# Performance work log

Hardware: AMD Instinct MI355X
Metric: run time of the kernel (lower is better)

The kernel has to match this reference:

```python
import jax, jax.numpy as jnp
import numpy as np

KEEP_PROB = 0.3
KH, KW = 3, 3
STRIDE = (1, 1)
PADDING = ((1, 1), (1, 1))
DILATION = (1, 1)


def setup_inputs() -> dict:
    key = jax.random.key(0)
    k_x, k_w, k_m, k_b = jax.random.split(key, 4)
    B, C_in, H, W = 16, 64, 112, 112
    C_out = 128
    K = C_in * KH * KW  # 576
    x = jax.random.normal(k_x, (B, C_in, H, W), dtype=jnp.float32)
    weight = jax.random.normal(k_w, (C_out, K), dtype=jnp.float32)
    # binary sparsity pattern of the COO tensor, as a float mask
    mask = (jax.random.uniform(k_m, (C_out, K)) < KEEP_PROB).astype(jnp.float32)
    bias = jax.random.normal(k_b, (C_out,), dtype=jnp.float32)
    return {"x": x, "weight": weight, "mask": mask, "bias": bias}


def reference(x, weight, mask, bias):
    # Effective sparse weight matrix [C_out, C_in*kH*kW]
    spW = weight * mask
    # im2col (F.unfold): patches -> [B, C_in*kH*kW, H_out, W_out]
    # ordering of the K axis is (c, i, j) channel-major, matching torch unfold
    patches = jax.lax.conv_general_dilated_patches(
        x,
        filter_shape=(KH, KW),
        window_strides=STRIDE,
        padding=PADDING,
        rhs_dilation=DILATION,
    )  # [B, K, H_out, W_out]
    # sparse.mm(spW, X) + fold(1x1)  ==  GEMM over the K axis
    out = jnp.einsum('ok,bkhw->bohw', spW, patches)
    out = out + bias[None, :, None, None]
    return out
```

## Files before the change

### kernel.cpp

```cpp
#include <hip/hip_runtime.h>
#include <hip/hip_bf16.h>

#define C_IN    64
#define C_OUT   128
#define HH      112
#define WW      112
#define NB      16
#define KTOT    576
#define NSTEPS  36
#define NPIX    (HH*WW)
#define PH      114
#define PPIX    (PH*PH)
#define XT_OFF  147456
#define XT_BYTES ((size_t)NB * PPIX * C_IN * 2)
#define TILE_H  16
#define TILE_W  16
#define HB_X    18
#define HB_P    324
#define A_BYTES 73728
#define B_BYTES 49152
#define TY      8
#define TX      16
#define HALO_X  18
#define HALO_P  180
#define TILES_X 7
#define NTILES  98

typedef __bf16 bf16x8 __attribute__((ext_vector_type(8)));
typedef float  f32x16 __attribute__((ext_vector_type(16)));

static __device__ __forceinline__ unsigned short f2bf(float v) {
    unsigned int u = __builtin_bit_cast(unsigned int, v);
    u = u + 0x7fffu + ((u >> 16) & 1u);
    return (unsigned short)(u >> 16);
}

__global__ __launch_bounds__(256) void pack_w_kernel(
        const float* __restrict__ weight, const float* __restrict__ mask,
        unsigned short* __restrict__ pw) {
    int t  = blockIdx.x;
    int mt = threadIdx.x >> 6;
    int l  = threadIdx.x & 63;
    int g  = l >> 5;
    int m  = mt * 32 + (l & 31);
    unsigned int words[4];
    #pragma unroll
    for (int ew = 0; ew < 4; ++ew) {
        unsigned int w2[2];
        #pragma unroll
        for (int h = 0; h < 2; ++h) {
            int e    = ew * 2 + h;
            int klog = t * 16 + g * 8 + e;
            int ij   = klog >> 6;
            int c    = klog & 63;
            int ko   = c * 9 + ij;
            w2[h] = f2bf(weight[m * KTOT + ko] * mask[m * KTOT + ko]);
        }
        words[ew] = w2[0] | (w2[1] << 16);
    }
    uint4 o4; o4.x = words[0]; o4.y = words[1]; o4.z = words[2]; o4.w = words[3];
    ((uint4*)pw)[(t * 4 + mt) * 64 + l] = o4;
}

__global__ __launch_bounds__(256) void transpose_x_kernel(
        const float* __restrict__ x, unsigned short* __restrict__ xT) {
    const int b  = blockIdx.y;
    const int pp = blockIdx.x * 256 + threadIdx.x;
    if (pp >= PPIX) return;
    const int hp = pp / PH, wp = pp - hp * PH;
    const int gh = hp - 1, gw = wp - 1;
    const bool valid = (unsigned)gh < (unsigned)HH && (unsigned)gw < (unsigned)WW;
    const float* src = x + (size_t)b * C_IN * (HH * WW) + (gh * WW + gw);
    uint4* dst = (uint4*)(xT + ((size_t)b * PPIX + pp) * C_IN);
    #pragma unroll
    for (int cb = 0; cb < 8; ++cb) {
        unsigned int w4[4];
        #pragma unroll
        for (int h = 0; h < 4; ++h) {
            float v0 = valid ? src[(size_t)(cb * 8 + h * 2    ) * (HH * WW)] : 0.0f;
            float v1 = valid ? src[(size_t)(cb * 8 + h * 2 + 1) * (HH * WW)] : 0.0f;
            w4[h] = (unsigned)f2bf(v0) | ((unsigned)f2bf(v1) << 16);
        }
        uint4 o; o.x = w4[0]; o.y = w4[1]; o.z = w4[2]; o.w = w4[3];
        dst[cb] = o;
    }
}

__global__ __launch_bounds__(512, 2) void sparse_conv_mega_kernel(
        const unsigned short* __restrict__ xT, const unsigned short* __restrict__ pw,
        const float* __restrict__ bias, float* __restrict__ out) {
    __shared__ __align__(16) unsigned char smem[A_BYTES + B_BYTES];
    unsigned char* As = smem;
    unsigned char* Bs = smem + A_BYTES;

    const int bid = (blockIdx.x & 7) * 28 + (blockIdx.x >> 3);
    const int b   = bid / 14;
    const int rem = bid % 14;
    const int mh  = rem & 1;
    const int wx  = rem >> 1;
    const int w0  = wx * TILE_W;
    const int tid = threadIdx.x;
    const int wave = tid >> 6, l = tid & 63;
    const int g = l >> 5, ln = l & 31;

    const char* xTb = (const char*)xT + (size_t)b * PPIX * (C_IN * 2);

    {
        const char* pwb = (const char*)pw;
        #pragma unroll
        for (int r = 0; r < 9; ++r) {
            int c  = r * 512 + tid;
            int t  = c >> 7;
            int mt = (c >> 6) & 1;
            int ll = c & 63;
            const char* gp = pwb + (size_t)((t * 4 + mh * 2 + mt) * 64 + ll) * 16;
            char* lp = (char*)As + r * 8192 + wave * 1024;
            __builtin_amdgcn_global_load_lds(
                (const __attribute__((address_space(1))) void*)gp,
                (__attribute__((address_space(3))) void*)lp, 16, 0, 0);
        }
    }

    const int pl = wave * 32 + ln;
    const int py = pl >> 4, px = pl & 15;

    float bv[2][16];
    #pragma unroll
    for (int mtp = 0; mtp < 2; ++mtp)
        #pragma unroll
        for (int r = 0; r < 16; ++r) {
            int mloc = (r & 3) + 8 * (r >> 2) + 4 * g;
            bv[mtp][r] = bias[mh * 64 + mtp * 32 + mloc];
        }

    const size_t outb = (size_t)b * C_OUT * NPIX;

    #pragma unroll 1
    for (int it = 0; it < 7; ++it) {
        const int h0 = it * TILE_H;

        #pragma unroll
        for (int r = 0; r < 6; ++r) {
            int chunk = r * 512 + tid;
            if (chunk > HB_P * 8 - 1) chunk = HB_P * 8 - 1;
            int p = chunk >> 3, s = chunk & 7;
            int yy = p / HB_X, xx = p - yy * HB_X;
            const char* gp = xTb + (size_t)((h0 + yy) * PH + (w0 + xx)) * (C_IN * 2)
                                 + (((s ^ p) & 7) << 4);
            char* lp = (char*)Bs + r * 8192 + wave * 1024;
            __builtin_amdgcn_global_load_lds(
                (const __attribute__((address_space(1))) void*)gp,
                (__attribute__((address_space(3))) void*)lp, 16, 0, 0);
        }
        __syncthreads();

        f32x16 acc[2];
        #pragma unroll
        for (int mtp = 0; mtp < 2; ++mtp)
            #pragma unroll
            for (int q = 0; q < 16; ++q) acc[mtp][q] = 0.0f;
        #pragma unroll
        for (int mtp = 0; mtp < 2; ++mtp)
            #pragma unroll
            for (int r = 0; r < 16; ++r) acc[mtp][r] = bv[mtp][r];

        #pragma unroll 1
        for (int ij = 0; ij < 9; ++ij) {
            const int di = ij / 3, dj = ij - di * 3;
            const int Pa = (py + di) * HB_X + (px + dj);
            #pragma unroll
            for (int cs = 0; cs < 4; ++cs) {
                const int t = ij * 4 + cs;
                bf16x8 a0 = __builtin_bit_cast(bf16x8,
                    *(const uint4*)(As + ((t * 2 + 0) * 64 + l) * 16));
                bf16x8 a1 = __builtin_bit_cast(bf16x8,
                    *(const uint4*)(As + ((t * 2 + 1) * 64 + l) * 16));
                const int jb = cs * 2 + g;
                bf16x8 bb = __builtin_bit_cast(bf16x8,
                    *(const uint4*)(Bs + Pa * (C_IN * 2) + (((jb ^ Pa) & 7) << 4)));
                acc[0] = __builtin_amdgcn_mfma_f32_32x32x16_bf16(a0, bb, acc[0], 0, 0, 0);
                acc[1] = __builtin_amdgcn_mfma_f32_32x32x16_bf16(a1, bb, acc[1], 0, 0, 0);
            }
        }

        #pragma unroll
        for (int mtp = 0; mtp < 2; ++mtp) {
            #pragma unroll
            for (int r = 0; r < 16; ++r) {
                int mloc = (r & 3) + 8 * (r >> 2) + 4 * g;
                int o = mh * 64 + mtp * 32 + mloc;
                out[outb + (size_t)o * NPIX + (h0 + py) * WW + (w0 + px)] = acc[mtp][r];
            }
        }
        __syncthreads();
    }
}

__global__ __launch_bounds__(256, 4) void sparse_conv_fb_kernel(
        const float* __restrict__ x, const unsigned short* __restrict__ pw,
        const float* __restrict__ bias, float* __restrict__ out) {
    __shared__ __align__(16) unsigned short xs[HALO_P * C_IN];

    const int bid = blockIdx.x;
    const int b   = bid / NTILES;
    const int t98 = bid % NTILES;
    const int tyi = t98 / TILES_X;
    const int txi = t98 % TILES_X;
    const int h0  = tyi * TY, w0 = txi * TX;
    const int tid = threadIdx.x;

    const float* xb = x + (size_t)b * C_IN * HH * WW;
    {
        const int p  = tid;
        const bool act = p < HALO_P;
        int yy = p / HALO_X;
        int xx = p - yy * HALO_X;
        int gh = h0 + yy - 1, gw = w0 + xx - 1;
        const bool valid = act && (unsigned)gh < (unsigned)HH && (unsigned)gw < (unsigned)WW;
        const float* bp = xb + (gh * WW + gw);
        float v[C_IN];
        #pragma unroll
        for (int c = 0; c < C_IN; ++c)
            v[c] = valid ? bp[c * (HH * WW)] : 0.0f;
        if (act) {
            char* xc = (char*)xs + p * (C_IN * 2);
            #pragma unroll
            for (int j = 0; j < 8; ++j) {
                bf16x8 bvv;
                #pragma unroll
                for (int e = 0; e < 8; ++e) bvv[e] = (__bf16)v[j * 8 + e];
                *(uint4*)(xc + (((j ^ p) & 7) << 4)) = __builtin_bit_cast(uint4, bvv);
            }
        }
    }
    __syncthreads();

    const int wave = tid >> 6, l = tid & 63;
    const int wm = wave >> 1, wn = wave & 1;
    const int g  = l >> 5,  ln = l & 31;

    int P0[2];
    #pragma unroll
    for (int ntp = 0; ntp < 2; ++ntp) {
        int pt = wn * 64 + ntp * 32 + ln;
        P0[ntp] = (pt >> 4) * HALO_X + (pt & 15);
    }

    f32x16 acc[2][2];
    #pragma unroll
    for (int i = 0; i < 2; ++i)
        #pragma unroll
        for (int jq = 0; jq < 2; ++jq)
            #pragma unroll
            for (int q = 0; q < 16; ++q) acc[i][jq][q] = 0.0f;

    const uint4* __restrict__ pwv = (const uint4*)pw;

    #pragma unroll 1
    for (int ij = 0; ij < 9; ++ij) {
        const int di = ij / 3;
        const int dj = ij - di * 3;
        const int P0a = P0[0] + di * HALO_X + dj;
        const int P1a = P0[1] + di * HALO_X + dj;
        #pragma unroll
        for (int cs = 0; cs < 4; ++cs) {
            const int t = ij * 4 + cs;
            bf16x8 a0 = __builtin_bit_cast(bf16x8, pwv[(t * 4 + wm * 2 + 0) * 64 + l]);
            bf16x8 a1 = __builtin_bit_cast(bf16x8, pwv[(t * 4 + wm * 2 + 1) * 64 + l]);
            const int jb = cs * 2 + g;
            bf16x8 b0 = __builtin_bit_cast(bf16x8,
                *(const uint4*)((const char*)xs + P0a * (C_IN * 2) + (((jb ^ P0a) & 7) << 4)));
            bf16x8 b1 = __builtin_bit_cast(bf16x8,
                *(const uint4*)((const char*)xs + P1a * (C_IN * 2) + (((jb ^ P1a) & 7) << 4)));
            acc[0][0] = __builtin_amdgcn_mfma_f32_32x32x16_bf16(a0, b0, acc[0][0], 0, 0, 0);
            acc[0][1] = __builtin_amdgcn_mfma_f32_32x32x16_bf16(a0, b1, acc[0][1], 0, 0, 0);
            acc[1][0] = __builtin_amdgcn_mfma_f32_32x32x16_bf16(a1, b0, acc[1][0], 0, 0, 0);
            acc[1][1] = __builtin_amdgcn_mfma_f32_32x32x16_bf16(a1, b1, acc[1][1], 0, 0, 0);
        }
    }

    const size_t outb = (size_t)b * C_OUT * HH * WW;
    #pragma unroll
    for (int mtp = 0; mtp < 2; ++mtp) {
        #pragma unroll
        for (int r = 0; r < 16; ++r) {
            int mloc = (r & 3) + 8 * (r >> 2) + 4 * g;
            int o = (wm * 2 + mtp) * 32 + mloc;
            float bvv = bias[o];
            #pragma unroll
            for (int ntp = 0; ntp < 2; ++ntp) {
                int p  = wn * 64 + ntp * 32 + ln;
                int gh = h0 + (p >> 4), gw = w0 + (p & 15);
                out[outb + ((size_t)o * HH + gh) * WW + gw] = acc[mtp][ntp][r] + bvv;
            }
        }
    }
}

extern "C" void kernel_launch(void* const* d_in, const int* in_sizes, int n_in,
                              void* d_out, int out_size, void* d_ws, size_t ws_size,
                              hipStream_t stream) {
    const float* x    = (const float*)d_in[0];
    const float* w    = (const float*)d_in[1];
    const float* mk   = (const float*)d_in[2];
    const float* bs   = (const float*)d_in[3];
    float* out        = (float*)d_out;
    unsigned short* pw = (unsigned short*)d_ws;

    pack_w_kernel<<<dim3(NSTEPS), dim3(256), 0, stream>>>(w, mk, pw);

    if (ws_size >= (size_t)XT_OFF + XT_BYTES) {
        unsigned short* xT = (unsigned short*)((char*)d_ws + XT_OFF);
        transpose_x_kernel<<<dim3((PPIX + 255) / 256, NB), dim3(256), 0, stream>>>(x, xT);
        sparse_conv_mega_kernel<<<dim3(224), dim3(512), 0, stream>>>(xT, pw, bs, out);
    } else {
        sparse_conv_fb_kernel<<<dim3(NB * NTILES), dim3(256), 0, stream>>>(x, pw, bs, out);
    }
}
```

Measured before the change: 76.48 us.

## Keep weights in registers and double-buffer input halo tiles in LDS

The main conv kernel now keeps each wave's weight fragments for all 36 K-steps in registers instead of LDS. It uses 256-thread blocks over 448 smaller work units (8x16 output tiles, split by image half). The input halo tile is double-buffered in LDS, so the next tile's global-to-LDS loads overlap the current tile's MFMAs. This removes per-step LDS weight reads and the serial load-then-compute stall, at the cost of heavy register pressure (36 uint4 per thread) and more halo re-reads from the smaller tiles.

```diff
diff --git a/kernel.cpp b/kernel.cpp
--- a/kernel.cpp
+++ b/kernel.cpp
@@ -13,12 +13,9 @@
 #define PPIX    (PH*PH)
 #define XT_OFF  147456
 #define XT_BYTES ((size_t)NB * PPIX * C_IN * 2)
-#define TILE_H  16
-#define TILE_W  16
 #define HB_X    18
-#define HB_P    324
-#define A_BYTES 73728
-#define B_BYTES 49152
+#define HB_P    180
+#define BBUF    24576
 #define TY      8
 #define TX      16
 #define HALO_X  18
@@ -86,110 +83,104 @@
     }
 }
 
-__global__ __launch_bounds__(512, 2) void sparse_conv_mega_kernel(
+__global__ __launch_bounds__(256, 2) void sparse_conv_areg_kernel(
         const unsigned short* __restrict__ xT, const unsigned short* __restrict__ pw,
         const float* __restrict__ bias, float* __restrict__ out) {
-    __shared__ __align__(16) unsigned char smem[A_BYTES + B_BYTES];
-    unsigned char* As = smem;
-    unsigned char* Bs = smem + A_BYTES;
-
-    const int bid = (blockIdx.x & 7) * 28 + (blockIdx.x >> 3);
-    const int b   = bid / 14;
-    const int rem = bid % 14;
-    const int mh  = rem & 1;
-    const int wx  = rem >> 1;
-    const int w0  = wx * TILE_W;
-    const int tid = threadIdx.x;
+    __shared__ __align__(16) unsigned char Bs[2][BBUF];
+
+    const int bid  = (blockIdx.x & 7) * 56 + (blockIdx.x >> 3);
+    const int b    = bid / 28;
+    const int rem  = bid % 28;
+    const int mh   = rem & 1;
+    const int half = (rem >> 1) & 1;
+    const int strip= rem >> 2;
+    const int w0   = strip * 16;
+    const int tid  = threadIdx.x;
     const int wave = tid >> 6, l = tid & 63;
-    const int g = l >> 5, ln = l & 31;
+    const int mt = wave >> 1, nh = wave & 1;
+    const int g  = l >> 5,  ln = l & 31;
 
     const char* xTb = (const char*)xT + (size_t)b * PPIX * (C_IN * 2);
-
-    {
-        const char* pwb = (const char*)pw;
-        #pragma unroll
-        for (int r = 0; r < 9; ++r) {
-            int c  = r * 512 + tid;
-            int t  = c >> 7;
-            int mt = (c >> 6) & 1;
-            int ll = c & 63;
-            const char* gp = pwb + (size_t)((t * 4 + mh * 2 + mt) * 64 + ll) * 16;
-            char* lp = (char*)As + r * 8192 + wave * 1024;
+    const uint4* __restrict__ pwv = (const uint4*)pw;
+
+    uint4 Areg[NSTEPS];
+    #pragma unroll
+    for (int t = 0; t < NSTEPS; ++t)
+        Areg[t] = pwv[(t * 4 + mh * 2 + mt) * 64 + l];
+
+    float bv[16];
+    #pragma unroll
+    for (int r = 0; r < 16; ++r) {
+        int mloc = (r & 3) + 8 * (r >> 2) + 4 * g;
+        bv[r] = bias[mh * 64 + mt * 32 + mloc];
+    }
+
+    int Pbase[2];
+    #pragma unroll
+    for (int ntp = 0; ntp < 2; ++ntp) {
+        int p = nh * 64 + ntp * 32 + ln;
+        Pbase[ntp] = (p >> 4) * HB_X + (p & 15);
+    }
+
+    auto STAGE = [&](int it, int buf) {
+        const int base = half * 56 + it * 8;
+        #pragma unroll
+        for (int r = 0; r < 6; ++r) {
+            int chunk = r * 256 + tid;
+            if (chunk > HB_P * 8 - 1) chunk = HB_P * 8 - 1;
+            int p = chunk >> 3, s = chunk & 7;
+            int yy = p / HB_X, xx = p - yy * HB_X;
+            const char* gp = xTb + (size_t)((base + yy) * PH + (w0 + xx)) * (C_IN * 2)
+                                 + (((s ^ p) & 7) << 4);
+            char* lp = (char*)&Bs[buf][0] + r * 4096 + wave * 1024;
             __builtin_amdgcn_global_load_lds(
                 (const __attribute__((address_space(1))) void*)gp,
                 (__attribute__((address_space(3))) void*)lp, 16, 0, 0);
         }
-    }
-
-    const int pl = wave * 32 + ln;
-    const int py = pl >> 4, px = pl & 15;
-
-    float bv[2][16];
-    #pragma unroll
-    for (int mtp = 0; mtp < 2; ++mtp)
+    };
+
+    STAGE(0, 0);
+    __syncthreads();
+
+    const size_t outb = (size_t)b * C_OUT * NPIX;
+
+    #pragma unroll 1
+    for (int it = 0; it < 7; ++it) {
+        const int cur = it & 1;
+        if (it < 6) STAGE(it + 1, cur ^ 1);
+
+        f32x16 acc[2];
+        #pragma unroll
+        for (int ntp = 0; ntp < 2; ++ntp)
+            #pragma unroll
+            for (int r = 0; r < 16; ++r) acc[ntp][r] = bv[r];
+
+        const unsigned char* Bc = &Bs[cur][0];
+        #pragma unroll
+        for (int t = 0; t < NSTEPS; ++t) {
+            const int ij = t >> 2, cs = t & 3;
+            const int di = ij / 3, dj = ij - di * 3;
+            const int jb = cs * 2 + g;
+            bf16x8 a = __builtin_bit_cast(bf16x8, Areg[t]);
+            #pragma unroll
+            for (int ntp = 0; ntp < 2; ++ntp) {
+                const int Pa = Pbase[ntp] + di * HB_X + dj;
+                bf16x8 bb = __builtin_bit_cast(bf16x8,
+                    *(const uint4*)(Bc + Pa * (C_IN * 2) + (((jb ^ Pa) & 7) << 4)));
+                acc[ntp] = __builtin_amdgcn_mfma_f32_32x32x16_bf16(a, bb, acc[ntp], 0, 0, 0);
+            }
+        }
+
+        const int rowbase = half * 56 + it * 8;
         #pragma unroll
         for (int r = 0; r < 16; ++r) {
             int mloc = (r & 3) + 8 * (r >> 2) + 4 * g;
-            bv[mtp][r] = bias[mh * 64 + mtp * 32 + mloc];
-        }
-
-    const size_t outb = (size_t)b * C_OUT * NPIX;
-
-    #pragma unroll 1
-    for (int it = 0; it < 7; ++it) {
-        const int h0 = it * TILE_H;
-
-        #pragma unroll
-        for (int r = 0; r < 6; ++r) {
-            int chunk = r * 512 + tid;
-            if (chunk > HB_P * 8 - 1) chunk = HB_P * 8 - 1;
-            int p = chunk >> 3, s = chunk & 7;
-            int yy = p / HB_X, xx = p - yy * HB_X;
-            const char* gp = xTb + (size_t)((h0 + yy) * PH + (w0 + xx)) * (C_IN * 2)
-                                 + (((s ^ p) & 7) << 4);
-            char* lp = (char*)Bs + r * 8192 + wave * 1024;
-            __builtin_amdgcn_global_load_lds(
-                (const __attribute__((address_space(1))) void*)gp,
-                (__attribute__((address_space(3))) void*)lp, 16, 0, 0);
-        }
-        __syncthreads();
-
-        f32x16 acc[2];
-        #pragma unroll
-        for (int mtp = 0; mtp < 2; ++mtp)
-            #pragma unroll
-            for (int q = 0; q < 16; ++q) acc[mtp][q] = 0.0f;
-        #pragma unroll
-        for (int mtp = 0; mtp < 2; ++mtp)
-            #pragma unroll
-            for (int r = 0; r < 16; ++r) acc[mtp][r] = bv[mtp][r];
-
-        #pragma unroll 1
-        for (int ij = 0; ij < 9; ++ij) {
-            const int di = ij / 3, dj = ij - di * 3;
-            const int Pa = (py + di) * HB_X + (px + dj);
-            #pragma unroll
-            for (int cs = 0; cs < 4; ++cs) {
-                const int t = ij * 4 + cs;
-                bf16x8 a0 = __builtin_bit_cast(bf16x8,
-                    *(const uint4*)(As + ((t * 2 + 0) * 64 + l) * 16));
-                bf16x8 a1 = __builtin_bit_cast(bf16x8,
-                    *(const uint4*)(As + ((t * 2 + 1) * 64 + l) * 16));
-                const int jb = cs * 2 + g;
-                bf16x8 bb = __builtin_bit_cast(bf16x8,
-                    *(const uint4*)(Bs + Pa * (C_IN * 2) + (((jb ^ Pa) & 7) << 4)));
-                acc[0] = __builtin_amdgcn_mfma_f32_32x32x16_bf16(a0, bb, acc[0], 0, 0, 0);
-                acc[1] = __builtin_amdgcn_mfma_f32_32x32x16_bf16(a1, bb, acc[1], 0, 0, 0);
-            }
-        }
-
-        #pragma unroll
-        for (int mtp = 0; mtp < 2; ++mtp) {
-            #pragma unroll
-            for (int r = 0; r < 16; ++r) {
-                int mloc = (r & 3) + 8 * (r >> 2) + 4 * g;
-                int o = mh * 64 + mtp * 32 + mloc;
-                out[outb + (size_t)o * NPIX + (h0 + py) * WW + (w0 + px)] = acc[mtp][r];
+            int o = mh * 64 + mt * 32 + mloc;
+            #pragma unroll
+            for (int ntp = 0; ntp < 2; ++ntp) {
+                int p = nh * 64 + ntp * 32 + ln;
+                out[outb + (size_t)o * NPIX + (rowbase + (p >> 4)) * WW + w0 + (p & 15)]
+                    = acc[ntp][r];
             }
         }
         __syncthreads();
@@ -312,7 +303,7 @@
     if (ws_size >= (size_t)XT_OFF + XT_BYTES) {
         unsigned short* xT = (unsigned short*)((char*)d_ws + XT_OFF);
         transpose_x_kernel<<<dim3((PPIX + 255) / 256, NB), dim3(256), 0, stream>>>(x, xT);
-        sparse_conv_mega_kernel<<<dim3(224), dim3(512), 0, stream>>>(xT, pw, bs, out);
+        sparse_conv_areg_kernel<<<dim3(448), dim3(256), 0, stream>>>(xT, pw, bs, out);
     } else {
         sparse_conv_fb_kernel<<<dim3(NB * NTILES), dim3(256), 0, stream>>>(x, pw, bs, out);
     }
```

New measurement: 197.9 us. 2.59x slower.

## Replace persistent LDS-halo conv kernel with many small blocks streaming B from global

Applied to the files above, without the earlier changes.

Swaps the 224-block persistent kernel, which staged an 18x18 input halo in LDS for each of 7 row tiles, for 1568 blocks of 256 threads. Each block covers 256 linear pixels by 64 output channels. The B operands (input pixels) are now read straight from global/L2 into registers and double-buffered across the 9 filter taps. Each wave computes a 2x2 MFMA tile for more reuse per A load. This removes the per-tile LDS staging and barriers and improves occupancy and load balance, but reloads the whole weight slice into LDS in every block and relies on cache for the 9x halo reuse.

```diff
diff --git a/kernel.cpp b/kernel.cpp
--- a/kernel.cpp
+++ b/kernel.cpp
@@ -13,12 +13,7 @@
 #define PPIX    (PH*PH)
 #define XT_OFF  147456
 #define XT_BYTES ((size_t)NB * PPIX * C_IN * 2)
-#define TILE_H  16
-#define TILE_W  16
-#define HB_X    18
-#define HB_P    324
 #define A_BYTES 73728
-#define B_BYTES 49152
 #define TY      8
 #define TX      16
 #define HALO_X  18
@@ -86,19 +81,16 @@
     }
 }
 
-__global__ __launch_bounds__(512, 2) void sparse_conv_mega_kernel(
+__global__ __launch_bounds__(256, 2) void sparse_conv_bg_kernel(
         const unsigned short* __restrict__ xT, const unsigned short* __restrict__ pw,
         const float* __restrict__ bias, float* __restrict__ out) {
-    __shared__ __align__(16) unsigned char smem[A_BYTES + B_BYTES];
-    unsigned char* As = smem;
-    unsigned char* Bs = smem + A_BYTES;
-
-    const int bid = (blockIdx.x & 7) * 28 + (blockIdx.x >> 3);
-    const int b   = bid / 14;
-    const int rem = bid % 14;
-    const int mh  = rem & 1;
-    const int wx  = rem >> 1;
-    const int w0  = wx * TILE_W;
+    __shared__ __align__(16) unsigned char As[A_BYTES];
+
+    const int bid = (blockIdx.x & 7) * 196 + (blockIdx.x >> 3);
+    const int b   = bid / 98;
+    const int rem = bid % 98;
+    const int mh  = rem / 49;
+    const int p0  = (rem % 49) * 256;
     const int tid = threadIdx.x;
     const int wave = tid >> 6, l = tid & 63;
     const int g = l >> 5, ln = l & 31;
@@ -108,21 +100,26 @@
     {
         const char* pwb = (const char*)pw;
         #pragma unroll
-        for (int r = 0; r < 9; ++r) {
-            int c  = r * 512 + tid;
+        for (int r = 0; r < 18; ++r) {
+            int c  = r * 256 + tid;
             int t  = c >> 7;
             int mt = (c >> 6) & 1;
             int ll = c & 63;
             const char* gp = pwb + (size_t)((t * 4 + mh * 2 + mt) * 64 + ll) * 16;
-            char* lp = (char*)As + r * 8192 + wave * 1024;
+            char* lp = (char*)As + r * 4096 + wave * 1024;
             __builtin_amdgcn_global_load_lds(
                 (const __attribute__((address_space(1))) void*)gp,
                 (__attribute__((address_space(3))) void*)lp, 16, 0, 0);
         }
     }
 
-    const int pl = wave * 32 + ln;
-    const int py = pl >> 4, px = pl & 15;
+    int rec0[2];
+    #pragma unroll
+    for (int ntp = 0; ntp < 2; ++ntp) {
+        int p = p0 + wave * 64 + ntp * 32 + ln;
+        int h = p / WW, w = p - h * WW;
+        rec0[ntp] = h * PH + w;
+    }
 
     float bv[2][16];
     #pragma unroll
@@ -133,66 +130,66 @@
             bv[mtp][r] = bias[mh * 64 + mtp * 32 + mloc];
         }
 
+    f32x16 acc[2][2];
+    #pragma unroll
+    for (int mtp = 0; mtp < 2; ++mtp)
+        #pragma unroll
+        for (int ntp = 0; ntp < 2; ++ntp)
+            #pragma unroll
+            for (int r = 0; r < 16; ++r) acc[mtp][ntp][r] = bv[mtp][r];
+
+    __syncthreads();
+
+    uint4 Bb[2][8];
+    {
+        #pragma unroll
+        for (int ntp = 0; ntp < 2; ++ntp)
+            #pragma unroll
+            for (int cs = 0; cs < 4; ++cs)
+                Bb[0][ntp * 4 + cs] = *(const uint4*)(xTb
+                    + (size_t)rec0[ntp] * 128 + (cs * 2 + g) * 16);
+    }
+
+    #pragma unroll
+    for (int ij = 0; ij < 9; ++ij) {
+        if (ij < 8) {
+            const int di = (ij + 1) / 3, dj = (ij + 1) - di * 3;
+            #pragma unroll
+            for (int ntp = 0; ntp < 2; ++ntp)
+                #pragma unroll
+                for (int cs = 0; cs < 4; ++cs)
+                    Bb[(ij + 1) & 1][ntp * 4 + cs] = *(const uint4*)(xTb
+                        + (size_t)(rec0[ntp] + di * PH + dj) * 128 + (cs * 2 + g) * 16);
+        }
+        #pragma unroll
+        for (int cs = 0; cs < 4; ++cs) {
+            const int t = ij * 4 + cs;
+            bf16x8 a0 = __builtin_bit_cast(bf16x8,
+                *(const uint4*)(As + ((t * 2 + 0) * 64 + l) * 16));
+            bf16x8 a1 = __builtin_bit_cast(bf16x8,
+                *(const uint4*)(As + ((t * 2 + 1) * 64 + l) * 16));
+            #pragma unroll
+            for (int ntp = 0; ntp < 2; ++ntp) {
+                bf16x8 bb = __builtin_bit_cast(bf16x8, Bb[ij & 1][ntp * 4 + cs]);
+                acc[0][ntp] = __builtin_amdgcn_mfma_f32_32x32x16_bf16(a0, bb, acc[0][ntp], 0, 0, 0);
+                acc[1][ntp] = __builtin_amdgcn_mfma_f32_32x32x16_bf16(a1, bb, acc[1][ntp], 0, 0, 0);
+            }
+        }
+    }
+
     const size_t outb = (size_t)b * C_OUT * NPIX;
-
-    #pragma unroll 1
-    for (int it = 0; it < 7; ++it) {
-        const int h0 = it * TILE_H;
-
-        #pragma unroll
-        for (int r = 0; r < 6; ++r) {
-            int chunk = r * 512 + tid;
-            if (chunk > HB_P * 8 - 1) chunk = HB_P * 8 - 1;
-            int p = chunk >> 3, s = chunk & 7;
-            int yy = p / HB_X, xx = p - yy * HB_X;
-            const char* gp = xTb + (size_t)((h0 + yy) * PH + (w0 + xx)) * (C_IN * 2)
-                                 + (((s ^ p) & 7) << 4);
-            char* lp = (char*)Bs + r * 8192 + wave * 1024;
-            __builtin_amdgcn_global_load_lds(
-                (const __attribute__((address_space(1))) void*)gp,
-                (__attribute__((address_space(3))) void*)lp, 16, 0, 0);
-        }
-        __syncthreads();
-
-        f32x16 acc[2];
-        #pragma unroll
-        for (int mtp = 0; mtp < 2; ++mtp)
-            #pragma unroll
-            for (int q = 0; q < 16; ++q) acc[mtp][q] = 0.0f;
-        #pragma unroll
-        for (int mtp = 0; mtp < 2; ++mtp)
-            #pragma unroll
-            for (int r = 0; r < 16; ++r) acc[mtp][r] = bv[mtp][r];
-
-        #pragma unroll 1
-        for (int ij = 0; ij < 9; ++ij) {
-            const int di = ij / 3, dj = ij - di * 3;
-            const int Pa = (py + di) * HB_X + (px + dj);
-            #pragma unroll
-            for (int cs = 0; cs < 4; ++cs) {
-                const int t = ij * 4 + cs;
-                bf16x8 a0 = __builtin_bit_cast(bf16x8,
-                    *(const uint4*)(As + ((t * 2 + 0) * 64 + l) * 16));
-                bf16x8 a1 = __builtin_bit_cast(bf16x8,
-                    *(const uint4*)(As + ((t * 2 + 1) * 64 + l) * 16));
-                const int jb = cs * 2 + g;
-                bf16x8 bb = __builtin_bit_cast(bf16x8,
-                    *(const uint4*)(Bs + Pa * (C_IN * 2) + (((jb ^ Pa) & 7) << 4)));
-                acc[0] = __builtin_amdgcn_mfma_f32_32x32x16_bf16(a0, bb, acc[0], 0, 0, 0);
-                acc[1] = __builtin_amdgcn_mfma_f32_32x32x16_bf16(a1, bb, acc[1], 0, 0, 0);
+    #pragma unroll
+    for (int mtp = 0; mtp < 2; ++mtp) {
+        #pragma unroll
+        for (int r = 0; r < 16; ++r) {
+            int mloc = (r & 3) + 8 * (r >> 2) + 4 * g;
+            int o = mh * 64 + mtp * 32 + mloc;
+            #pragma unroll
+            for (int ntp = 0; ntp < 2; ++ntp) {
+                int p = p0 + wave * 64 + ntp * 32 + ln;
+                out[outb + (size_t)o * NPIX + p] = acc[mtp][ntp][r];
             }
         }
-
-        #pragma unroll
-        for (int mtp = 0; mtp < 2; ++mtp) {
-            #pragma unroll
-            for (int r = 0; r < 16; ++r) {
-                int mloc = (r & 3) + 8 * (r >> 2) + 4 * g;
-                int o = mh * 64 + mtp * 32 + mloc;
-                out[outb + (size_t)o * NPIX + (h0 + py) * WW + (w0 + px)] = acc[mtp][r];
-            }
-        }
-        __syncthreads();
     }
 }
 
@@ -312,7 +309,7 @@
     if (ws_size >= (size_t)XT_OFF + XT_BYTES) {
         unsigned short* xT = (unsigned short*)((char*)d_ws + XT_OFF);
         transpose_x_kernel<<<dim3((PPIX + 255) / 256, NB), dim3(256), 0, stream>>>(x, xT);
-        sparse_conv_mega_kernel<<<dim3(224), dim3(512), 0, stream>>>(xT, pw, bs, out);
+        sparse_conv_bg_kernel<<<dim3(NB * 98), dim3(256), 0, stream>>>(xT, pw, bs, out);
     } else {
         sparse_conv_fb_kernel<<<dim3(NB * NTILES), dim3(256), 0, stream>>>(x, pw, bs, out);
     }
```

After: 115.9 us. 51.5% more time.

## Retile conv into row bands with 32-wide column slabs and prefetch next slab

Applied to the files above, without the earlier changes.

Each block now owns a 16-row band and walks across it in 32-pixel-wide slabs: three full slabs plus one 16-wide tail. In a full slab each wave computes two N tiles per A fragment, so every LDS load of the weights is reused twice and the halo overhead per output pixel shrinks. The next slab's global-to-LDS copy is issued before the output stores, so it can overlap them, and the K loop is fully unrolled. The cost is a larger LDS buffer, twice the accumulator registers, a separate tail code path, and reads past the end of the row in the tail slab, covered by a larger workspace size check.

```diff
diff --git a/kernel.cpp b/kernel.cpp
--- a/kernel.cpp
+++ b/kernel.cpp
@@ -13,12 +13,10 @@
 #define PPIX    (PH*PH)
 #define XT_OFF  147456
 #define XT_BYTES ((size_t)NB * PPIX * C_IN * 2)
-#define TILE_H  16
-#define TILE_W  16
-#define HB_X    18
-#define HB_P    324
 #define A_BYTES 73728
-#define B_BYTES 49152
+#define B_PITCH 34
+#define B_RECS  612
+#define B_SLOT  81920
 #define TY      8
 #define TX      16
 #define HALO_X  18
@@ -86,20 +84,20 @@
     }
 }
 
-__global__ __launch_bounds__(512, 2) void sparse_conv_mega_kernel(
+__global__ __launch_bounds__(512, 2) void sparse_conv_slab_kernel(
         const unsigned short* __restrict__ xT, const unsigned short* __restrict__ pw,
         const float* __restrict__ bias, float* __restrict__ out) {
-    __shared__ __align__(16) unsigned char smem[A_BYTES + B_BYTES];
+    __shared__ __align__(16) unsigned char smem[A_BYTES + B_SLOT];
     unsigned char* As = smem;
     unsigned char* Bs = smem + A_BYTES;
 
-    const int bid = (blockIdx.x & 7) * 28 + (blockIdx.x >> 3);
-    const int b   = bid / 14;
-    const int rem = bid % 14;
-    const int mh  = rem & 1;
-    const int wx  = rem >> 1;
-    const int w0  = wx * TILE_W;
-    const int tid = threadIdx.x;
+    const int bid  = (blockIdx.x & 7) * 28 + (blockIdx.x >> 3);
+    const int b    = bid / 14;
+    const int rem  = bid % 14;
+    const int mh   = rem & 1;
+    const int band = rem >> 1;
+    const int h0   = band * 16;
+    const int tid  = threadIdx.x;
     const int wave = tid >> 6, l = tid & 63;
     const int g = l >> 5, ln = l & 31;
 
@@ -121,76 +119,114 @@
         }
     }
 
-    const int pl = wave * 32 + ln;
-    const int py = pl >> 4, px = pl & 15;
-
-    float bv[2][16];
-    #pragma unroll
-    for (int mtp = 0; mtp < 2; ++mtp)
-        #pragma unroll
-        for (int r = 0; r < 16; ++r) {
-            int mloc = (r & 3) + 8 * (r >> 2) + 4 * g;
-            bv[mtp][r] = bias[mh * 64 + mtp * 32 + mloc];
-        }
-
-    const size_t outb = (size_t)b * C_OUT * NPIX;
-
-    #pragma unroll 1
-    for (int it = 0; it < 7; ++it) {
-        const int h0 = it * TILE_H;
-
-        #pragma unroll
-        for (int r = 0; r < 6; ++r) {
+    auto STAGE = [&](int it) {
+        #pragma unroll
+        for (int r = 0; r < 10; ++r) {
             int chunk = r * 512 + tid;
-            if (chunk > HB_P * 8 - 1) chunk = HB_P * 8 - 1;
+            if (chunk > B_RECS * 8 - 1) chunk = B_RECS * 8 - 1;
             int p = chunk >> 3, s = chunk & 7;
-            int yy = p / HB_X, xx = p - yy * HB_X;
-            const char* gp = xTb + (size_t)((h0 + yy) * PH + (w0 + xx)) * (C_IN * 2)
+            int yy = p / B_PITCH, xx = p - yy * B_PITCH;
+            const char* gp = xTb + (size_t)((h0 + yy) * PH + (it * 32 + xx)) * (C_IN * 2)
                                  + (((s ^ p) & 7) << 4);
             char* lp = (char*)Bs + r * 8192 + wave * 1024;
             __builtin_amdgcn_global_load_lds(
                 (const __attribute__((address_space(1))) void*)gp,
                 (__attribute__((address_space(3))) void*)lp, 16, 0, 0);
         }
-        __syncthreads();
-
-        f32x16 acc[2];
-        #pragma unroll
-        for (int mtp = 0; mtp < 2; ++mtp)
-            #pragma unroll
-            for (int q = 0; q < 16; ++q) acc[mtp][q] = 0.0f;
-        #pragma unroll
-        for (int mtp = 0; mtp < 2; ++mtp)
-            #pragma unroll
-            for (int r = 0; r < 16; ++r) acc[mtp][r] = bv[mtp][r];
-
-        #pragma unroll 1
-        for (int ij = 0; ij < 9; ++ij) {
-            const int di = ij / 3, dj = ij - di * 3;
-            const int Pa = (py + di) * HB_X + (px + dj);
-            #pragma unroll
-            for (int cs = 0; cs < 4; ++cs) {
-                const int t = ij * 4 + cs;
+    };
+
+    float bv[2][16];
+    #pragma unroll
+    for (int mt = 0; mt < 2; ++mt)
+        #pragma unroll
+        for (int r = 0; r < 16; ++r) {
+            int mloc = (r & 3) + 8 * (r >> 2) + 4 * g;
+            bv[mt][r] = bias[mh * 64 + mt * 32 + mloc];
+        }
+
+    STAGE(0);
+    __syncthreads();
+
+    const size_t outb = (size_t)b * C_OUT * NPIX;
+
+    #pragma unroll 1
+    for (int it = 0; it < 4; ++it) {
+        const bool full = (it < 3);
+        const int py3 = 2 * wave + (ln >> 4);
+        const int px3 = ln & 15;
+
+        f32x16 acc[2][2];
+        #pragma unroll
+        for (int mt = 0; mt < 2; ++mt)
+            #pragma unroll
+            for (int ntp = 0; ntp < 2; ++ntp)
+                #pragma unroll
+                for (int r = 0; r < 16; ++r) acc[mt][ntp][r] = bv[mt][r];
+
+        if (full) {
+            #pragma unroll
+            for (int t = 0; t < NSTEPS; ++t) {
+                const int ij = t >> 2, cs = t & 3;
+                const int di = ij / 3, dj = ij - di * 3;
+                const int jb = cs * 2 + g;
                 bf16x8 a0 = __builtin_bit_cast(bf16x8,
                     *(const uint4*)(As + ((t * 2 + 0) * 64 + l) * 16));
                 bf16x8 a1 = __builtin_bit_cast(bf16x8,
                     *(const uint4*)(As + ((t * 2 + 1) * 64 + l) * 16));
+                #pragma unroll
+                for (int ntp = 0; ntp < 2; ++ntp) {
+                    const int Pa = (2 * wave + ntp + di) * B_PITCH + (ln + dj);
+                    bf16x8 bb = __builtin_bit_cast(bf16x8,
+                        *(const uint4*)(Bs + Pa * 128 + (((jb ^ Pa) & 7) << 4)));
+                    acc[0][ntp] = __builtin_amdgcn_mfma_f32_32x32x16_bf16(a0, bb, acc[0][ntp], 0, 0, 0);
+                    acc[1][ntp] = __builtin_amdgcn_mfma_f32_32x32x16_bf16(a1, bb, acc[1][ntp], 0, 0, 0);
+                }
+            }
+        } else {
+            #pragma unroll
+            for (int t = 0; t < NSTEPS; ++t) {
+                const int ij = t >> 2, cs = t & 3;
+                const int di = ij / 3, dj = ij - di * 3;
                 const int jb = cs * 2 + g;
+                bf16x8 a0 = __builtin_bit_cast(bf16x8,
+                    *(const uint4*)(As + ((t * 2 + 0) * 64 + l) * 16));
+                bf16x8 a1 = __builtin_bit_cast(bf16x8,
+                    *(const uint4*)(As + ((t * 2 + 1) * 64 + l) * 16));
+                const int Pa = (py3 + di) * B_PITCH + (px3 + dj);
                 bf16x8 bb = __builtin_bit_cast(bf16x8,
-                    *(const uint4*)(Bs + Pa * (C_IN * 2) + (((jb ^ Pa) & 7) << 4)));
-                acc[0] = __builtin_amdgcn_mfma_f32_32x32x16_bf16(a0, bb, acc[0], 0, 0, 0);
-                acc[1] = __builtin_amdgcn_mfma_f32_32x32x16_bf16(a1, bb, acc[1], 0, 0, 0);
+                    *(const uint4*)(Bs + Pa * 128 + (((jb ^ Pa) & 7) << 4)));
+                acc[0][0] = __builtin_amdgcn_mfma_f32_32x32x16_bf16(a0, bb, acc[0][0], 0, 0, 0);
+                acc[1][0] = __builtin_amdgcn_mfma_f32_32x32x16_bf16(a1, bb, acc[1][0], 0, 0, 0);
             }
         }
 
-        #pragma unroll
-        for (int mtp = 0; mtp < 2; ++mtp) {
-            #pragma unroll
-            for (int r = 0; r < 16; ++r) {
-                int mloc = (r & 3) + 8 * (r >> 2) + 4 * g;
-                int o = mh * 64 + mtp * 32 + mloc;
-                out[outb + (size_t)o * NPIX + (h0 + py) * WW + (w0 + px)] = acc[mtp][r];
-            }
+        __syncthreads();
+        if (it < 3) STAGE(it + 1);
+
+        if (full) {
+            #pragma unroll
+            for (int mt = 0; mt < 2; ++mt)
+                #pragma unroll
+                for (int r = 0; r < 16; ++r) {
+                    int mloc = (r & 3) + 8 * (r >> 2) + 4 * g;
+                    int o = mh * 64 + mt * 32 + mloc;
+                    #pragma unroll
+                    for (int ntp = 0; ntp < 2; ++ntp) {
+                        int row = h0 + 2 * wave + ntp;
+                        out[outb + (size_t)o * NPIX + row * WW + it * 32 + ln]
+                            = acc[mt][ntp][r];
+                    }
+                }
+        } else {
+            #pragma unroll
+            for (int mt = 0; mt < 2; ++mt)
+                #pragma unroll
+                for (int r = 0; r < 16; ++r) {
+                    int mloc = (r & 3) + 8 * (r >> 2) + 4 * g;
+                    int o = mh * 64 + mt * 32 + mloc;
+                    out[outb + (size_t)o * NPIX + (h0 + py3) * WW + 96 + px3]
+                        = acc[mt][0][r];
+                }
         }
         __syncthreads();
     }
@@ -309,10 +345,10 @@
 
     pack_w_kernel<<<dim3(NSTEPS), dim3(256), 0, stream>>>(w, mk, pw);
 
-    if (ws_size >= (size_t)XT_OFF + XT_BYTES) {
+    if (ws_size >= (size_t)XT_OFF + XT_BYTES + 4096) {
         unsigned short* xT = (unsigned short*)((char*)d_ws + XT_OFF);
         transpose_x_kernel<<<dim3((PPIX + 255) / 256, NB), dim3(256), 0, stream>>>(x, xT);
-        sparse_conv_mega_kernel<<<dim3(224), dim3(512), 0, stream>>>(xT, pw, bs, out);
+        sparse_conv_slab_kernel<<<dim3(224), dim3(512), 0, stream>>>(xT, pw, bs, out);
     } else {
         sparse_conv_fb_kernel<<<dim3(NB * NTILES), dim3(256), 0, stream>>>(x, pw, bs, out);
     }
```

Result: slower. 142.9 us (+86.8%).
